# Kernel tuning notes

Hardware: AMD Instinct MI355X
Metric: run time of the kernel (lower is better)

The kernel has to match this reference:

```python
import jax, jax.numpy as jnp
import numpy as np

MUL_S, MUL_V = 64, 32                     # multiplicities of 0e and 1o irreps
FEAT_DIM = MUL_S + 3 * MUL_V              # 160
V_NODES, N_NODES = 2000, 200000
AVG_NODES = 100.0
SQRT3 = float(np.sqrt(3.0))
FAN_TP = 96.0                             # sum over TP paths of mul1*mul2 feeding each output irrep (64+32)
SILU_NORM = 1.6790590                     # e3nn normalize2mom constant for SiLU (E[silu(x)^2]^-0.5, x~N(0,1))


def _split(x):
    # x: [N, 160] -> scalars [N,64], vectors [N,32,3]
    return x[:, :MUL_S], x[:, MUL_S:].reshape(x.shape[0], MUL_V, 3)


def _merge(s, v):
    return jnp.concatenate([s, v.reshape(v.shape[0], 3 * MUL_V)], axis=1)


def _o3_linear(x, Ws, Wv):
    # e3nn o3.Linear: per-irrep channel mixing with 1/sqrt(fan_in) path normalization
    s, v = _split(x)
    s2 = (s @ Ws) / np.sqrt(float(MUL_S))
    v2 = jnp.einsum('nui,uv->nvi', v, Wv) / np.sqrt(float(MUL_V))
    return s2, v2


def _act(s, v):
    # e3nn Activation: SiLU (normalized) on 0e scalars, identity on l>0
    return jax.nn.silu(s) * SILU_NORM, v


def _fc_tp(x, sh, WA, WB, WC, WD):
    # FullyConnectedTensorProduct((64x0e+32x1o) x (1x0e+1x1o) -> 64x0e+32x1o)
    # Paths: 0e*0e->0e (WA), 1o.1o->0e (WB, w3j=delta/sqrt3),
    #        1o*0e->1o (WC, w3j=delta/sqrt3 absorbed via /sqrt3), 0e*1o->1o (WD, /sqrt3)
    s, v = _split(x)
    sh0, sh1 = sh[:, :1], sh[:, 1:]                     # [N,1], [N,3]
    dot = jnp.einsum('nui,ni->nu', v, sh1) / SQRT3      # [N,32]
    out_s = ((s * sh0) @ WA + dot @ WB) / np.sqrt(FAN_TP)
    out_v = (jnp.einsum('nui,uv->nvi', v * sh0[:, :, None], WC)
             + jnp.einsum('nu,ni,uv->nvi', s, sh1, WD)) / (SQRT3 * np.sqrt(FAN_TP))
    return out_s, out_v


def setup_inputs() -> dict:
    key = jax.random.key(0)
    ks = jax.random.split(key, 14)
    return {
        'x_virtual': jax.random.normal(ks[0], (V_NODES, FEAT_DIM), jnp.float32),
        'x_node': jax.random.normal(ks[1], (N_NODES, FEAT_DIM), jnp.float32),
        'node_pos_sh': jax.random.normal(ks[2], (N_NODES, 4), jnp.float32),
        'Ws_vsc': jax.random.normal(ks[3], (MUL_S, MUL_S), jnp.float32),
        'Wv_vsc': jax.random.normal(ks[4], (MUL_V, MUL_V), jnp.float32),
        'Ws_nsc': jax.random.normal(ks[5], (MUL_S, MUL_S), jnp.float32),
        'Wv_nsc': jax.random.normal(ks[6], (MUL_V, MUL_V), jnp.float32),
        'WA': jax.random.normal(ks[7], (MUL_S, MUL_S), jnp.float32),
        'WB': jax.random.normal(ks[8], (MUL_V, MUL_S), jnp.float32),
        'WC': jax.random.normal(ks[9], (MUL_V, MUL_V), jnp.float32),
        'WD': jax.random.normal(ks[10], (MUL_S, MUL_V), jnp.float32),
        'Ws_n2v': jax.random.normal(ks[11], (MUL_S, MUL_S), jnp.float32),
        'Wv_n2v': jax.random.normal(ks[12], (MUL_V, MUL_V), jnp.float32),
        'batch': jnp.sort(jax.random.randint(ks[13], (N_NODES,), 0, V_NODES)),
    }


def reference(x_virtual, x_node, node_pos_sh, Ws_vsc, Wv_vsc, Ws_nsc, Wv_nsc,
              WA, WB, WC, WD, Ws_n2v, Wv_n2v, batch):
    # self-connections
    sv_s, sv_v = _o3_linear(x_virtual, Ws_vsc, Wv_vsc)
    sn_s, sn_v = _o3_linear(x_node, Ws_nsc, Wv_nsc)
    # node -> virtual messages via equivariant tensor product + scatter_add
    m_s, m_v = _fc_tp(x_node, node_pos_sh, WA, WB, WC, WD)
    m_s = jax.ops.segment_sum(m_s, batch, num_segments=V_NODES) / np.sqrt(AVG_NODES)
    m_v = jax.ops.segment_sum(m_v, batch, num_segments=V_NODES) / np.sqrt(AVG_NODES)
    m_s, m_v = _act(m_s, m_v)
    xv_s = (sv_s + m_s) / np.sqrt(2.0)
    xv_v = (sv_v + m_v) / np.sqrt(2.0)
    x_virtual_out = _merge(xv_s, xv_v)
    # virtual -> node: gather, linear, activation
    g = x_virtual_out[batch]
    gn_s, gn_v = _o3_linear(g, Ws_n2v, Wv_n2v)
    gn_s, gn_v = _act(gn_s, gn_v)
    xn_s = (sn_s + gn_s) / np.sqrt(2.0)
    xn_v = (sn_v + gn_v) / np.sqrt(2.0)
    return x_virtual_out, _merge(xn_s, xn_v)
```

## Files before the change

kernel.cpp:

```cpp
#include <hip/hip_runtime.h>
#include <math.h>

#define MUL_S 64
#define MUL_V 32
#define FEAT  160
#define VN    2000
#define NN    200000
#define NGRP16 (NN / 16)
#define XSTR  168

#define INV8         0.125f
#define INV_SQRT32   0.17677669529663687f
#define INV_SQRT3    0.57735026918962576f
#define INV_SQRT96   0.10206207261596575f
#define INV_S3S96    0.05892556509887896f
#define INV_SQRT2    0.70710678118654752f
#define INV_SQRT_AVG 0.1f

typedef __attribute__((ext_vector_type(8))) short bf16x8;
typedef __attribute__((ext_vector_type(4))) float f32x4;

#define MFMA(a, b, c) __builtin_amdgcn_mfma_f32_16x16x32_bf16((a), (b), (c), 0, 0, 0)

__device__ __forceinline__ short f2bf(float f) {
    union { float f; unsigned u; } c; c.f = f;
    unsigned r = c.u + 0x7FFFu + ((c.u >> 16) & 1u);
    return (short)(r >> 16);
}
__device__ __forceinline__ float bf2f(short s) {
    union { unsigned u; float f; } c; c.u = ((unsigned)(unsigned short)s) << 16;
    return c.f;
}
__device__ __forceinline__ float silu_n(float x) {
    return x * (1.0f / (1.0f + __expf(-x))) * 1.679059f;
}

__device__ __forceinline__ bf16x8 load_bfrag(const float* __restrict__ W, int N,
                                             int kbase, int col, int lhi) {
    const float* p = W + (size_t)(kbase + lhi * 8) * N + col;
    bf16x8 b;
#pragma unroll
    for (int e = 0; e < 8; ++e) b[e] = f2bf(p[(size_t)e * N]);
    return b;
}

__global__ __launch_bounds__(64) void k1_msg(
    const float* __restrict__ x_node, const float* __restrict__ sh,
    const float* __restrict__ WA, const float* __restrict__ WB,
    const float* __restrict__ WC, const float* __restrict__ WD,
    const int* __restrict__ batch, float* __restrict__ m_acc)
{
    __shared__ short xbf[16 * XSTR] __attribute__((aligned(16)));
    __shared__ float mt[16][FEAT + 1];
    __shared__ float shs[16][4];
    __shared__ int   bs[16];

    const int lane = threadIdx.x;
    const int lrow = lane & 15, lhi = lane >> 4;

    bf16x8 bWA[4][2], bWB[4], bWC[2], bWD[2][2];
#pragma unroll
    for (int nt = 0; nt < 4; ++nt) {
        bWA[nt][0] = load_bfrag(WA, 64, 0,  lrow + 16 * nt, lhi);
        bWA[nt][1] = load_bfrag(WA, 64, 32, lrow + 16 * nt, lhi);
        bWB[nt]    = load_bfrag(WB, 64, 0,  lrow + 16 * nt, lhi);
    }
#pragma unroll
    for (int nt = 0; nt < 2; ++nt) {
        bWC[nt]    = load_bfrag(WC, 32, 0,  lrow + 16 * nt, lhi);
        bWD[nt][0] = load_bfrag(WD, 32, 0,  lrow + 16 * nt, lhi);
        bWD[nt][1] = load_bfrag(WD, 32, 32, lrow + 16 * nt, lhi);
    }

    for (int g0 = blockIdx.x; g0 < NGRP16; g0 += gridDim.x) {
        const int n0 = g0 * 16;
        __builtin_amdgcn_sched_barrier(0);

        if (lane < 16) bs[lane] = batch[n0 + lane];
        shs[lane >> 2][lane & 3] = sh[(size_t)n0 * 4 + lane];
        {
            const float4* xb4 = (const float4*)(x_node + (size_t)n0 * FEAT);
#pragma unroll
            for (int it = 0; it < 10; ++it) {
                int i4 = lane + it * 64;
                float4 v = xb4[i4];
                int row = i4 / 40;
                int c0  = (i4 - row * 40) * 4;
                if (c0 < MUL_S) {
                    short4 s4;
                    s4.x = f2bf(v.x); s4.y = f2bf(v.y); s4.z = f2bf(v.z); s4.w = f2bf(v.w);
                    *(short4*)&xbf[row * XSTR + c0] = s4;
                } else {
                    int t = c0 - MUL_S;
                    xbf[row * XSTR + MUL_S + ((t + 0) % 3) * 32 + (t + 0) / 3] = f2bf(v.x);
                    xbf[row * XSTR + MUL_S + ((t + 1) % 3) * 32 + (t + 1) / 3] = f2bf(v.y);
                    xbf[row * XSTR + MUL_S + ((t + 2) % 3) * 32 + (t + 2) / 3] = f2bf(v.z);
                    xbf[row * XSTR + MUL_S + ((t + 3) % 3) * 32 + (t + 3) / 3] = f2bf(v.w);
                }
            }
        }
        __builtin_amdgcn_sched_barrier(0);

        const int arow = lrow * XSTR + lhi * 8;
        bf16x8 aS0 = *(const bf16x8*)&xbf[arow];
        bf16x8 aS1 = *(const bf16x8*)&xbf[arow + 32];
        bf16x8 aV0 = *(const bf16x8*)&xbf[arow + 64];
        bf16x8 aV1 = *(const bf16x8*)&xbf[arow + 96];
        bf16x8 aV2 = *(const bf16x8*)&xbf[arow + 128];
        bf16x8 aDot;
        {
            float s1a = shs[lrow][1], s1b = shs[lrow][2], s1c = shs[lrow][3];
#pragma unroll
            for (int e = 0; e < 8; ++e)
                aDot[e] = f2bf((bf2f(aV0[e]) * s1a + bf2f(aV1[e]) * s1b +
                                bf2f(aV2[e]) * s1c) * INV_SQRT3);
        }

        f32x4 accA[4], accB[4], accD[2], accC0[2], accC1[2], accC2[2];
#pragma unroll
        for (int nt = 0; nt < 4; ++nt) { accA[nt] = (f32x4){0,0,0,0}; accB[nt] = (f32x4){0,0,0,0}; }
#pragma unroll
        for (int nt = 0; nt < 2; ++nt) { accD[nt] = (f32x4){0,0,0,0};
            accC0[nt] = (f32x4){0,0,0,0}; accC1[nt] = (f32x4){0,0,0,0}; accC2[nt] = (f32x4){0,0,0,0}; }

#pragma unroll
        for (int nt = 0; nt < 4; ++nt) {
            accA[nt] = MFMA(aS0, bWA[nt][0], accA[nt]);
            accA[nt] = MFMA(aS1, bWA[nt][1], accA[nt]);
            accB[nt] = MFMA(aDot, bWB[nt], accB[nt]);
        }
#pragma unroll
        for (int nt = 0; nt < 2; ++nt) {
            accD[nt]  = MFMA(aS0, bWD[nt][0], accD[nt]);
            accD[nt]  = MFMA(aS1, bWD[nt][1], accD[nt]);
            accC0[nt] = MFMA(aV0, bWC[nt], accC0[nt]);
            accC1[nt] = MFMA(aV1, bWC[nt], accC1[nt]);
            accC2[nt] = MFMA(aV2, bWC[nt], accC2[nt]);
        }

        float sh0q[4], sh1q[4][3];
#pragma unroll
        for (int q = 0; q < 4; ++q) {
            int rr = lhi * 4 + q;
            sh0q[q] = shs[rr][0];
            sh1q[q][0] = shs[rr][1]; sh1q[q][1] = shs[rr][2]; sh1q[q][2] = shs[rr][3];
        }
#pragma unroll
        for (int nt = 0; nt < 4; ++nt)
#pragma unroll
            for (int q = 0; q < 4; ++q)
                mt[lhi * 4 + q][16 * nt + lrow] =
                    (accA[nt][q] * sh0q[q] + accB[nt][q]) * INV_SQRT96;
#pragma unroll
        for (int nt = 0; nt < 2; ++nt)
#pragma unroll
            for (int q = 0; q < 4; ++q) {
                int w = 16 * nt + lrow, rr = lhi * 4 + q;
                float td = accD[nt][q];
                mt[rr][MUL_S + 3 * w + 0] = (accC0[nt][q] * sh0q[q] + td * sh1q[q][0]) * INV_S3S96;
                mt[rr][MUL_S + 3 * w + 1] = (accC1[nt][q] * sh0q[q] + td * sh1q[q][1]) * INV_S3S96;
                mt[rr][MUL_S + 3 * w + 2] = (accC2[nt][q] * sh0q[q] + td * sh1q[q][2]) * INV_S3S96;
            }
        __builtin_amdgcn_sched_barrier(0);

        for (int c = lane; c < FEAT; c += 64) {
            float run = mt[0][c];
            int bprev = bs[0];
#pragma unroll
            for (int k = 1; k < 16; ++k) {
                int b = bs[k];
                if (b != bprev) {
                    atomicAdd(&m_acc[(size_t)bprev * FEAT + c], run);
                    run = 0.f; bprev = b;
                }
                run += mt[k][c];
            }
            atomicAdd(&m_acc[(size_t)bprev * FEAT + c], run);
        }
    }
}

__global__ __launch_bounds__(256) void phase2(
    const float* __restrict__ x_virtual,
    const float* __restrict__ Ws_vsc, const float* __restrict__ Wv_vsc,
    const float* __restrict__ m_acc,
    float* __restrict__ out_virtual)
{
    __shared__ float xs[32][FEAT + 4];
    const int block0 = blockIdx.x * 32;
    for (int idx = threadIdx.x; idx < 32 * FEAT; idx += 256) {
        int r = idx / FEAT, c = idx - r * FEAT;
        int n = block0 + r;
        xs[r][c] = (n < VN) ? x_virtual[(size_t)n * FEAT + c] : 0.f;
    }
    __syncthreads();
    const int r = threadIdx.x >> 3, g = threadIdx.x & 7, n = block0 + r;
    if (n >= VN) return;

    float acc_s[8] = {};
    for (int k = 0; k < MUL_S; ++k) {
        float xv = xs[r][k];
        const float* wrow = Ws_vsc + k * MUL_S + g * 8;
#pragma unroll
        for (int jj = 0; jj < 8; ++jj) acc_s[jj] = fmaf(xv, wrow[jj], acc_s[jj]);
    }
    float acc_v[4][3] = {};
    for (int u = 0; u < MUL_V; ++u) {
        float v0 = xs[r][MUL_S + 3 * u], v1 = xs[r][MUL_S + 3 * u + 1], v2 = xs[r][MUL_S + 3 * u + 2];
        const float* wrow = Wv_vsc + u * MUL_V + g * 4;
#pragma unroll
        for (int ww = 0; ww < 4; ++ww) {
            float wv = wrow[ww];
            acc_v[ww][0] = fmaf(v0, wv, acc_v[ww][0]);
            acc_v[ww][1] = fmaf(v1, wv, acc_v[ww][1]);
            acc_v[ww][2] = fmaf(v2, wv, acc_v[ww][2]);
        }
    }
    const float* mrow = m_acc + (size_t)n * FEAT;
    float* outrow = out_virtual + (size_t)n * FEAT;
#pragma unroll
    for (int jj = 0; jj < 8; ++jj) {
        int j = g * 8 + jj;
        outrow[j] = (acc_s[jj] * INV8 + silu_n(mrow[j] * INV_SQRT_AVG)) * INV_SQRT2;
    }
#pragma unroll
    for (int ww = 0; ww < 4; ++ww)
#pragma unroll
        for (int i = 0; i < 3; ++i) {
            int cc = MUL_S + (g * 4 + ww) * 3 + i;
            outrow[cc] = (acc_v[ww][i] * INV_SQRT32 + mrow[cc] * INV_SQRT_AVG) * INV_SQRT2;
        }
}

__global__ __launch_bounds__(256, 2) void k2_out(
    const float* __restrict__ x_node, const float* __restrict__ out_virtual,
    const float* __restrict__ Ws_nsc, const float* __restrict__ Wv_nsc,
    const float* __restrict__ Ws_n2v, const float* __restrict__ Wv_n2v,
    const int* __restrict__ batch, float* __restrict__ out_node)
{
    __shared__ short xbf[64 * XSTR] __attribute__((aligned(16)));
    __shared__ short gbf[64 * XSTR] __attribute__((aligned(16)));
    __shared__ int   bs[64];

    const int lane = threadIdx.x & 63;
    const int lrow = lane & 15, lhi = lane >> 4;
    const int r0 = (threadIdx.x >> 6) * 16;

    bf16x8 bS1[4][2], bV1[2], bS2[4][2], bV2[2];
#pragma unroll
    for (int nt = 0; nt < 4; ++nt) {
        bS1[nt][0] = load_bfrag(Ws_nsc, 64, 0,  lrow + 16 * nt, lhi);
        bS1[nt][1] = load_bfrag(Ws_nsc, 64, 32, lrow + 16 * nt, lhi);
        bS2[nt][0] = load_bfrag(Ws_n2v, 64, 0,  lrow + 16 * nt, lhi);
        bS2[nt][1] = load_bfrag(Ws_n2v, 64, 32, lrow + 16 * nt, lhi);
    }
#pragma unroll
    for (int nt = 0; nt < 2; ++nt) {
        bV1[nt] = load_bfrag(Wv_nsc, 32, 0, lrow + 16 * nt, lhi);
        bV2[nt] = load_bfrag(Wv_n2v, 32, 0, lrow + 16 * nt, lhi);
    }

    for (int g0 = blockIdx.x; g0 < NN / 64; g0 += gridDim.x) {
        const int n0 = g0 * 64;
        __syncthreads();
        if (threadIdx.x < 64) bs[threadIdx.x] = batch[n0 + threadIdx.x];
        __syncthreads();
#pragma unroll 8
        for (int it = 0; it < 40; ++it) {
            int idx = threadIdx.x + it * 256;
            int row = idx / FEAT, col = idx - row * FEAT;
            int t = col - MUL_S;
            int dc = (col < MUL_S) ? col : MUL_S + (t % 3) * 32 + t / 3;
            xbf[row * XSTR + dc] = f2bf(x_node[(size_t)n0 * FEAT + idx]);
            gbf[row * XSTR + dc] = f2bf(out_virtual[(size_t)bs[row] * FEAT + col]);
        }
        __syncthreads();

        const int arow = (r0 + lrow) * XSTR + lhi * 8;
        bf16x8 axS0 = *(const bf16x8*)&xbf[arow];
        bf16x8 axS1 = *(const bf16x8*)&xbf[arow + 32];
        bf16x8 axV0 = *(const bf16x8*)&xbf[arow + 64];
        bf16x8 axV1 = *(const bf16x8*)&xbf[arow + 96];
        bf16x8 axV2 = *(const bf16x8*)&xbf[arow + 128];
        bf16x8 agS0 = *(const bf16x8*)&gbf[arow];
        bf16x8 agS1 = *(const bf16x8*)&gbf[arow + 32];
        bf16x8 agV0 = *(const bf16x8*)&gbf[arow + 64];
        bf16x8 agV1 = *(const bf16x8*)&gbf[arow + 96];
        bf16x8 agV2 = *(const bf16x8*)&gbf[arow + 128];

#pragma unroll
        for (int nt = 0; nt < 4; ++nt) {
            f32x4 sa = (f32x4){0,0,0,0}, ga = (f32x4){0,0,0,0};
            sa = MFMA(axS0, bS1[nt][0], sa); sa = MFMA(axS1, bS1[nt][1], sa);
            ga = MFMA(agS0, bS2[nt][0], ga); ga = MFMA(agS1, bS2[nt][1], ga);
#pragma unroll
            for (int q = 0; q < 4; ++q) {
                int gr = n0 + r0 + lhi * 4 + q;
                out_node[(size_t)gr * FEAT + 16 * nt + lrow] =
                    (sa[q] * INV8 + silu_n(ga[q] * INV8)) * INV_SQRT2;
            }
        }
#pragma unroll
        for (int nt = 0; nt < 2; ++nt) {
            f32x4 s0 = (f32x4){0,0,0,0}, s1 = (f32x4){0,0,0,0}, s2 = (f32x4){0,0,0,0};
            f32x4 g0v = (f32x4){0,0,0,0}, g1 = (f32x4){0,0,0,0}, g2 = (f32x4){0,0,0,0};
            s0 = MFMA(axV0, bV1[nt], s0); s1 = MFMA(axV1, bV1[nt], s1); s2 = MFMA(axV2, bV1[nt], s2);
            g0v = MFMA(agV0, bV2[nt], g0v); g1 = MFMA(agV1, bV2[nt], g1); g2 = MFMA(agV2, bV2[nt], g2);
            const float sc = INV_SQRT32 * INV_SQRT2;
#pragma unroll
            for (int q = 0; q < 4; ++q) {
                int gr = n0 + r0 + lhi * 4 + q;
                int w = 16 * nt + lrow;
                float* op = out_node + (size_t)gr * FEAT + MUL_S + 3 * w;
                op[0] = (s0[q] + g0v[q]) * sc;
                op[1] = (s1[q] + g1[q]) * sc;
                op[2] = (s2[q] + g2[q]) * sc;
            }
        }
    }
}

extern "C" void kernel_launch(void* const* d_in, const int* in_sizes, int n_in,
                              void* d_out, int out_size, void* d_ws, size_t ws_size,
                              hipStream_t stream)
{
    const float* x_virtual = (const float*)d_in[0];
    const float* x_node    = (const float*)d_in[1];
    const float* sh        = (const float*)d_in[2];
    const float* Ws_vsc    = (const float*)d_in[3];
    const float* Wv_vsc    = (const float*)d_in[4];
    const float* Ws_nsc    = (const float*)d_in[5];
    const float* Wv_nsc    = (const float*)d_in[6];
    const float* WA        = (const float*)d_in[7];
    const float* WB        = (const float*)d_in[8];
    const float* WC        = (const float*)d_in[9];
    const float* WD        = (const float*)d_in[10];
    const float* Ws_n2v    = (const float*)d_in[11];
    const float* Wv_n2v    = (const float*)d_in[12];
    const int*   batch     = (const int*)d_in[13];

    float* out         = (float*)d_out;
    float* out_virtual = out;
    float* out_node    = out + VN * FEAT;
    float* m_acc       = (float*)d_ws;

    hipMemsetAsync(m_acc, 0, (size_t)VN * FEAT * sizeof(float), stream);

    k1_msg<<<2560, 64, 0, stream>>>(x_node, sh, WA, WB, WC, WD, batch, m_acc);
    phase2<<<(VN + 31) / 32, 256, 0, stream>>>(x_virtual, Ws_vsc, Wv_vsc,
                                               m_acc, out_virtual);
    k2_out<<<512, 256, 0, stream>>>(x_node, out_virtual, Ws_nsc, Wv_nsc,
                                    Ws_n2v, Wv_n2v, batch, out_node);
}
```

Measured before the change: 149.9 us.

## Load MFMA fragments directly from global memory and reduce segments in registers

The message kernel stops staging x_node, sh and batch through shared memory. Each lane now loads its own A-fragment data straight from global memory, applies sh0 before the bf16 conversion, and builds the dot-product fragment in registers. When all 16 rows of a group share one batch id, the scatter becomes a cross-lane shuffle reduction followed by a single atomic per column; otherwise a per-lane 4-row segmented run is used. This removes the LDS round trips and cuts atomic traffic, at the cost of less coalesced, strided global loads and more atomics in mixed groups. The grid is also reduced from 2560 to 2048 blocks.

```diff
diff --git a/kernel.cpp b/kernel.cpp
--- a/kernel.cpp
+++ b/kernel.cpp
@@ -50,11 +50,6 @@
     const float* __restrict__ WC, const float* __restrict__ WD,
     const int* __restrict__ batch, float* __restrict__ m_acc)
 {
-    __shared__ short xbf[16 * XSTR] __attribute__((aligned(16)));
-    __shared__ float mt[16][FEAT + 1];
-    __shared__ float shs[16][4];
-    __shared__ int   bs[16];
-
     const int lane = threadIdx.x;
     const int lrow = lane & 15, lhi = lane >> 4;
 
@@ -74,108 +69,133 @@
 
     for (int g0 = blockIdx.x; g0 < NGRP16; g0 += gridDim.x) {
         const int n0 = g0 * 16;
-        __builtin_amdgcn_sched_barrier(0);
-
-        if (lane < 16) bs[lane] = batch[n0 + lane];
-        shs[lane >> 2][lane & 3] = sh[(size_t)n0 * 4 + lane];
-        {
-            const float4* xb4 = (const float4*)(x_node + (size_t)n0 * FEAT);
-#pragma unroll
-            for (int it = 0; it < 10; ++it) {
-                int i4 = lane + it * 64;
-                float4 v = xb4[i4];
-                int row = i4 / 40;
-                int c0  = (i4 - row * 40) * 4;
-                if (c0 < MUL_S) {
-                    short4 s4;
-                    s4.x = f2bf(v.x); s4.y = f2bf(v.y); s4.z = f2bf(v.z); s4.w = f2bf(v.w);
-                    *(short4*)&xbf[row * XSTR + c0] = s4;
-                } else {
-                    int t = c0 - MUL_S;
-                    xbf[row * XSTR + MUL_S + ((t + 0) % 3) * 32 + (t + 0) / 3] = f2bf(v.x);
-                    xbf[row * XSTR + MUL_S + ((t + 1) % 3) * 32 + (t + 1) / 3] = f2bf(v.y);
-                    xbf[row * XSTR + MUL_S + ((t + 2) % 3) * 32 + (t + 2) / 3] = f2bf(v.z);
-                    xbf[row * XSTR + MUL_S + ((t + 3) % 3) * 32 + (t + 3) / 3] = f2bf(v.w);
+        const float* xrow = x_node + (size_t)(n0 + lrow) * FEAT;
+
+        float4 xq0 = *(const float4*)(xrow + lhi * 8);
+        float4 xq1 = *(const float4*)(xrow + lhi * 8 + 4);
+        float4 xq2 = *(const float4*)(xrow + 32 + lhi * 8);
+        float4 xq3 = *(const float4*)(xrow + 32 + lhi * 8 + 4);
+        float4 vq0 = *(const float4*)(xrow + 64 + 24 * lhi);
+        float4 vq1 = *(const float4*)(xrow + 64 + 24 * lhi + 4);
+        float4 vq2 = *(const float4*)(xrow + 64 + 24 * lhi + 8);
+        float4 vq3 = *(const float4*)(xrow + 64 + 24 * lhi + 12);
+        float4 vq4 = *(const float4*)(xrow + 64 + 24 * lhi + 16);
+        float4 vq5 = *(const float4*)(xrow + 64 + 24 * lhi + 20);
+        float4 shr = *(const float4*)(sh + (size_t)(n0 + lrow) * 4);
+        float4 sh4[4];
+#pragma unroll
+        for (int q = 0; q < 4; ++q)
+            sh4[q] = *(const float4*)(sh + (size_t)(n0 + lhi * 4 + q) * 4);
+        const int b_lo = batch[n0];
+        const int b_hi = batch[n0 + 15];
+        const int4 bq4 = *(const int4*)(batch + n0 + lhi * 4);
+
+        const float sh0 = shr.x;
+        float vf[24];
+        *(float4*)&vf[0]  = vq0; *(float4*)&vf[4]  = vq1;
+        *(float4*)&vf[8]  = vq2; *(float4*)&vf[12] = vq3;
+        *(float4*)&vf[16] = vq4; *(float4*)&vf[20] = vq5;
+
+        bf16x8 aS0, aS1, aS0s, aS1s, aV0s, aV1s, aV2s, aDot;
+#pragma unroll
+        for (int e = 0; e < 4; ++e) {
+            float a = (&xq0.x)[e], b = (&xq1.x)[e];
+            float c = (&xq2.x)[e], d = (&xq3.x)[e];
+            aS0[e]     = f2bf(a);        aS0[e + 4] = f2bf(b);
+            aS1[e]     = f2bf(c);        aS1[e + 4] = f2bf(d);
+            aS0s[e]    = f2bf(a * sh0);  aS0s[e + 4] = f2bf(b * sh0);
+            aS1s[e]    = f2bf(c * sh0);  aS1s[e + 4] = f2bf(d * sh0);
+        }
+#pragma unroll
+        for (int e = 0; e < 8; ++e) {
+            float v0 = vf[3 * e], v1 = vf[3 * e + 1], v2 = vf[3 * e + 2];
+            aV0s[e] = f2bf(v0 * sh0);
+            aV1s[e] = f2bf(v1 * sh0);
+            aV2s[e] = f2bf(v2 * sh0);
+            aDot[e] = f2bf((v0 * shr.y + v1 * shr.z + v2 * shr.w) * INV_SQRT3);
+        }
+
+        f32x4 accS[4], accD[2], accC[2][3];
+#pragma unroll
+        for (int nt = 0; nt < 4; ++nt) {
+            f32x4 a = MFMA(aDot, bWB[nt], ((f32x4){0.f, 0.f, 0.f, 0.f}));
+            a = MFMA(aS0s, bWA[nt][0], a);
+            a = MFMA(aS1s, bWA[nt][1], a);
+            accS[nt] = a;
+        }
+#pragma unroll
+        for (int nt = 0; nt < 2; ++nt) {
+            f32x4 d = MFMA(aS1, bWD[nt][1], ((f32x4){0.f, 0.f, 0.f, 0.f}));
+            d = MFMA(aS0, bWD[nt][0], d);
+            accD[nt] = d;
+            accC[nt][0] = MFMA(aV0s, bWC[nt], ((f32x4){0.f, 0.f, 0.f, 0.f}));
+            accC[nt][1] = MFMA(aV1s, bWC[nt], ((f32x4){0.f, 0.f, 0.f, 0.f}));
+            accC[nt][2] = MFMA(aV2s, bWC[nt], ((f32x4){0.f, 0.f, 0.f, 0.f}));
+        }
+
+        if (b_lo == b_hi) {
+#pragma unroll
+            for (int nt = 0; nt < 4; ++nt) {
+                float s = (accS[nt][0] + accS[nt][1] + accS[nt][2] + accS[nt][3])
+                          * INV_SQRT96;
+                s += __shfl_xor(s, 16, 64);
+                s += __shfl_xor(s, 32, 64);
+                if (lhi == 0)
+                    atomicAdd(&m_acc[(size_t)b_lo * FEAT + 16 * nt + lrow], s);
+            }
+#pragma unroll
+            for (int nt = 0; nt < 2; ++nt)
+#pragma unroll
+                for (int i = 0; i < 3; ++i) {
+                    float s = 0.f;
+#pragma unroll
+                    for (int q = 0; q < 4; ++q)
+                        s += accC[nt][i][q] + accD[nt][q] * (&sh4[q].y)[i];
+                    s *= INV_S3S96;
+                    s += __shfl_xor(s, 16, 64);
+                    s += __shfl_xor(s, 32, 64);
+                    if (lhi == 0)
+                        atomicAdd(&m_acc[(size_t)b_lo * FEAT + MUL_S
+                                         + 3 * (16 * nt + lrow) + i], s);
                 }
+        } else {
+            const int bqa[4] = { bq4.x, bq4.y, bq4.z, bq4.w };
+#pragma unroll
+            for (int nt = 0; nt < 4; ++nt) {
+                const int col = 16 * nt + lrow;
+                float run = accS[nt][0] * INV_SQRT96;
+                int bp = bqa[0];
+#pragma unroll
+                for (int q = 1; q < 4; ++q) {
+                    float v = accS[nt][q] * INV_SQRT96;
+                    if (bqa[q] != bp) {
+                        atomicAdd(&m_acc[(size_t)bp * FEAT + col], run);
+                        run = 0.f; bp = bqa[q];
+                    }
+                    run += v;
+                }
+                atomicAdd(&m_acc[(size_t)bp * FEAT + col], run);
             }
-        }
-        __builtin_amdgcn_sched_barrier(0);
-
-        const int arow = lrow * XSTR + lhi * 8;
-        bf16x8 aS0 = *(const bf16x8*)&xbf[arow];
-        bf16x8 aS1 = *(const bf16x8*)&xbf[arow + 32];
-        bf16x8 aV0 = *(const bf16x8*)&xbf[arow + 64];
-        bf16x8 aV1 = *(const bf16x8*)&xbf[arow + 96];
-        bf16x8 aV2 = *(const bf16x8*)&xbf[arow + 128];
-        bf16x8 aDot;
-        {
-            float s1a = shs[lrow][1], s1b = shs[lrow][2], s1c = shs[lrow][3];
-#pragma unroll
-            for (int e = 0; e < 8; ++e)
-                aDot[e] = f2bf((bf2f(aV0[e]) * s1a + bf2f(aV1[e]) * s1b +
-                                bf2f(aV2[e]) * s1c) * INV_SQRT3);
-        }
-
-        f32x4 accA[4], accB[4], accD[2], accC0[2], accC1[2], accC2[2];
-#pragma unroll
-        for (int nt = 0; nt < 4; ++nt) { accA[nt] = (f32x4){0,0,0,0}; accB[nt] = (f32x4){0,0,0,0}; }
-#pragma unroll
-        for (int nt = 0; nt < 2; ++nt) { accD[nt] = (f32x4){0,0,0,0};
-            accC0[nt] = (f32x4){0,0,0,0}; accC1[nt] = (f32x4){0,0,0,0}; accC2[nt] = (f32x4){0,0,0,0}; }
-
-#pragma unroll
-        for (int nt = 0; nt < 4; ++nt) {
-            accA[nt] = MFMA(aS0, bWA[nt][0], accA[nt]);
-            accA[nt] = MFMA(aS1, bWA[nt][1], accA[nt]);
-            accB[nt] = MFMA(aDot, bWB[nt], accB[nt]);
-        }
-#pragma unroll
-        for (int nt = 0; nt < 2; ++nt) {
-            accD[nt]  = MFMA(aS0, bWD[nt][0], accD[nt]);
-            accD[nt]  = MFMA(aS1, bWD[nt][1], accD[nt]);
-            accC0[nt] = MFMA(aV0, bWC[nt], accC0[nt]);
-            accC1[nt] = MFMA(aV1, bWC[nt], accC1[nt]);
-            accC2[nt] = MFMA(aV2, bWC[nt], accC2[nt]);
-        }
-
-        float sh0q[4], sh1q[4][3];
-#pragma unroll
-        for (int q = 0; q < 4; ++q) {
-            int rr = lhi * 4 + q;
-            sh0q[q] = shs[rr][0];
-            sh1q[q][0] = shs[rr][1]; sh1q[q][1] = shs[rr][2]; sh1q[q][2] = shs[rr][3];
-        }
-#pragma unroll
-        for (int nt = 0; nt < 4; ++nt)
-#pragma unroll
-            for (int q = 0; q < 4; ++q)
-                mt[lhi * 4 + q][16 * nt + lrow] =
-                    (accA[nt][q] * sh0q[q] + accB[nt][q]) * INV_SQRT96;
-#pragma unroll
-        for (int nt = 0; nt < 2; ++nt)
-#pragma unroll
-            for (int q = 0; q < 4; ++q) {
-                int w = 16 * nt + lrow, rr = lhi * 4 + q;
-                float td = accD[nt][q];
-                mt[rr][MUL_S + 3 * w + 0] = (accC0[nt][q] * sh0q[q] + td * sh1q[q][0]) * INV_S3S96;
-                mt[rr][MUL_S + 3 * w + 1] = (accC1[nt][q] * sh0q[q] + td * sh1q[q][1]) * INV_S3S96;
-                mt[rr][MUL_S + 3 * w + 2] = (accC2[nt][q] * sh0q[q] + td * sh1q[q][2]) * INV_S3S96;
-            }
-        __builtin_amdgcn_sched_barrier(0);
-
-        for (int c = lane; c < FEAT; c += 64) {
-            float run = mt[0][c];
-            int bprev = bs[0];
-#pragma unroll
-            for (int k = 1; k < 16; ++k) {
-                int b = bs[k];
-                if (b != bprev) {
-                    atomicAdd(&m_acc[(size_t)bprev * FEAT + c], run);
-                    run = 0.f; bprev = b;
+#pragma unroll
+            for (int nt = 0; nt < 2; ++nt)
+#pragma unroll
+                for (int i = 0; i < 3; ++i) {
+                    const int col = MUL_S + 3 * (16 * nt + lrow) + i;
+                    float run = (accC[nt][i][0] + accD[nt][0] * (&sh4[0].y)[i])
+                                * INV_S3S96;
+                    int bp = bqa[0];
+#pragma unroll
+                    for (int q = 1; q < 4; ++q) {
+                        float v = (accC[nt][i][q] + accD[nt][q] * (&sh4[q].y)[i])
+                                  * INV_S3S96;
+                        if (bqa[q] != bp) {
+                            atomicAdd(&m_acc[(size_t)bp * FEAT + col], run);
+                            run = 0.f; bp = bqa[q];
+                        }
+                        run += v;
+                    }
+                    atomicAdd(&m_acc[(size_t)bp * FEAT + col], run);
                 }
-                run += mt[k][c];
-            }
-            atomicAdd(&m_acc[(size_t)bprev * FEAT + c], run);
         }
     }
 }
@@ -346,7 +366,7 @@
 
     hipMemsetAsync(m_acc, 0, (size_t)VN * FEAT * sizeof(float), stream);
 
-    k1_msg<<<2560, 64, 0, stream>>>(x_node, sh, WA, WB, WC, WD, batch, m_acc);
+    k1_msg<<<2048, 64, 0, stream>>>(x_node, sh, WA, WB, WC, WD, batch, m_acc);
     phase2<<<(VN + 31) / 32, 256, 0, stream>>>(x_virtual, Ws_vsc, Wv_vsc,
                                                m_acc, out_virtual);
     k2_out<<<512, 256, 0, stream>>>(x_node, out_virtual, Ws_nsc, Wv_nsc,
```

Result: faster. 121.8 us, median of 2 (-18.7%).
